# Kernel optimization log

Measured on AMD Instinct MI355X. Metric: run time of the kernel, lower is better.

The kernel has to match this reference:

```python
import jax, jax.numpy as jnp
import numpy as np

B, Q, K, DIM, H = 16, 256, 4096, 1024, 16
HD = DIM // H          # head_dim = 64
SCALE = float(np.sqrt(HD))
MAX_QUERIES = 64       # keep_first=True -> kept Q' = MAX_QUERIES + 1


def setup_inputs() -> dict:
    key = jax.random.key(0)
    ks = jax.random.split(key, 8)
    s = 1.0 / np.sqrt(DIM)
    return {
        "q": jax.random.normal(ks[0], (B, Q, DIM), jnp.float32),
        "k": jax.random.normal(ks[1], (B, K, DIM), jnp.float32),
        "v": jax.random.normal(ks[2], (B, K, DIM), jnp.float32),
        "Wq": jax.random.normal(ks[3], (DIM, DIM), jnp.float32) * s,
        "Wk": jax.random.normal(ks[4], (DIM, DIM), jnp.float32) * s,
        "Wv": jax.random.normal(ks[5], (DIM, DIM), jnp.float32) * s,
        "Wo": jax.random.normal(ks[6], (DIM, DIM), jnp.float32) * s,
        "bo": jnp.zeros((DIM,), jnp.float32),
    }


def _split_heads(x):  # [B, L, DIM] -> [B, L, H, HD]
    return x.reshape(x.shape[0], x.shape[1], H, HD)


def reference(q, k, v, Wq, Wk, Wv, Wo, bo):
    # QKV projections (no bias, matching qkv_bias=False; torch Linear is x @ W.T)
    qh = _split_heads(q @ Wq.T)   # [B,Q,H,HD]
    kh = _split_heads(k @ Wk.T)   # [B,K,H,HD]
    vh = _split_heads(v @ Wv.T)   # [B,K,H,HD]

    dots = jnp.einsum("bqhc,bkhc->bhqk", qh / SCALE, kh)  # [B,H,Q,K]

    # select_queries with keep_first=True: stats on detached dots over queries 1:
    sg = jax.lax.stop_gradient(dots)[:, :, 1:, :]          # [B,H,Q-1,K]
    stats = jax.nn.softmax(sg, axis=-2)                    # softmax over query axis
    score = stats.max(axis=(1, 3))                         # amax over (H, K) -> [B, Q-1]
    _, idx = jax.lax.top_k(score, MAX_QUERIES)             # [B, MAX_QUERIES]
    keep = jnp.concatenate(
        [jnp.zeros((dots.shape[0], 1), idx.dtype), idx + 1], axis=-1
    )                                                      # [B, Q'] with Q' = MAX_QUERIES+1

    dots_sel = jnp.take_along_axis(dots, keep[:, None, :, None], axis=2)  # [B,H,Q',K]

    # Competitive softmax: normalize over the (kept) query axis
    attn = jax.nn.softmax(dots_sel, axis=2)                # [B,H,Q',K]

    out = jnp.einsum("bhqk,bkhc->bqhc", attn, vh)          # [B,Q',H,HD]
    out = out.reshape(out.shape[0], out.shape[1], DIM)     # [B,Q',DIM]
    out = out @ Wo.T + bo
    return out, keep
```

## Files before the change

kernel.cpp:

```cpp
#include <hip/hip_runtime.h>
#include <hip/hip_bf16.h>
#include <math.h>

#define B_ 16
#define Q_ 256
#define K_ 4096
#define DIM_ 1024
#define H_ 16
#define HD_ 64
#define MQ_ 64
#define QP_ 65
#define SCALE_INV 0.125f

typedef unsigned short u16;
typedef __attribute__((ext_vector_type(8))) short bf16x8;
typedef __attribute__((ext_vector_type(8))) _Float16 f16x8;
typedef __attribute__((ext_vector_type(8))) short s16x8;
typedef __attribute__((ext_vector_type(4))) float f32x4;

__device__ __forceinline__ u16 f2bf_rne(float f) {
  unsigned u = __float_as_uint(f);
  u += 0x7fffu + ((u >> 16) & 1u);
  return (u16)(u >> 16);
}
__device__ __forceinline__ float bf2f(u16 h) {
  return __uint_as_float(((unsigned)h) << 16);
}
__device__ __forceinline__ u16 f2h_bits(float f) {
  _Float16 h = (_Float16)f;
  return *(u16*)&h;
}
__device__ __forceinline__ f16x8 as_f16x8(s16x8 v) {
  return __builtin_bit_cast(f16x8, v);
}
__device__ __forceinline__ void gload16(const void* g, void* l) {
  __builtin_amdgcn_global_load_lds(
      (const __attribute__((address_space(1))) unsigned int*)g,
      (__attribute__((address_space(3))) unsigned int*)l, 16, 0, 0);
}

__global__ __launch_bounds__(256) void split_bf16(
    const float* __restrict__ x, u16* __restrict__ hi, u16* __restrict__ lo,
    long n8, int wlo) {
  long i = (long)blockIdx.x * 256 + threadIdx.x;
  const long stride = (long)gridDim.x * 256;
  for (; i < n8; i += stride) {
    const float4 a = ((const float4*)x)[2 * i];
    const float4 b = ((const float4*)x)[2 * i + 1];
    const float xs[8] = {a.x, a.y, a.z, a.w, b.x, b.y, b.z, b.w};
    u16 h[8], l[8];
#pragma unroll
    for (int j = 0; j < 8; ++j) {
      h[j] = f2bf_rne(xs[j]);
      l[j] = f2bf_rne(xs[j] - bf2f(h[j]));
    }
    uint4 hv;
    hv.x = h[0] | ((unsigned)h[1] << 16);
    hv.y = h[2] | ((unsigned)h[3] << 16);
    hv.z = h[4] | ((unsigned)h[5] << 16);
    hv.w = h[6] | ((unsigned)h[7] << 16);
    ((uint4*)hi)[i] = hv;
    if (wlo) {
      uint4 lv;
      lv.x = l[0] | ((unsigned)l[1] << 16);
      lv.y = l[2] | ((unsigned)l[3] << 16);
      lv.z = l[4] | ((unsigned)l[5] << 16);
      lv.w = l[6] | ((unsigned)l[7] << 16);
      ((uint4*)lo)[i] = lv;
    }
  }
}

__global__ __launch_bounds__(256) void split_f16(
    const float* __restrict__ x, u16* __restrict__ hi, u16* __restrict__ lo,
    long n8) {
  long i = (long)blockIdx.x * 256 + threadIdx.x;
  const long stride = (long)gridDim.x * 256;
  for (; i < n8; i += stride) {
    const float4 a = ((const float4*)x)[2 * i];
    const float4 b = ((const float4*)x)[2 * i + 1];
    const float xs[8] = {a.x, a.y, a.z, a.w, b.x, b.y, b.z, b.w};
    u16 h[8], l[8];
#pragma unroll
    for (int j = 0; j < 8; ++j) {
      _Float16 hh = (_Float16)xs[j];
      _Float16 ll = (_Float16)(xs[j] - (float)hh);
      h[j] = *(u16*)&hh;
      l[j] = *(u16*)&ll;
    }
    uint4 hv;
    hv.x = h[0] | ((unsigned)h[1] << 16);
    hv.y = h[2] | ((unsigned)h[3] << 16);
    hv.z = h[4] | ((unsigned)h[5] << 16);
    hv.w = h[6] | ((unsigned)h[7] << 16);
    ((uint4*)hi)[i] = hv;
    uint4 lv;
    lv.x = l[0] | ((unsigned)l[1] << 16);
    lv.y = l[2] | ((unsigned)l[3] << 16);
    lv.z = l[4] | ((unsigned)l[5] << 16);
    lv.w = l[6] | ((unsigned)l[7] << 16);
    ((uint4*)lo)[i] = lv;
  }
}

template <int NPROD, int OUTM>
__global__ __launch_bounds__(256) void mfma_gemm(
    const u16* __restrict__ Ahp, const u16* __restrict__ Alp,
    const u16* __restrict__ Bhp, const u16* __restrict__ Blp,
    float* __restrict__ C, u16* __restrict__ ChH, u16* __restrict__ ChL) {
  __shared__ u16 Ah_s[128 * 32];
  __shared__ u16 Bh_s[128 * 32];
  __shared__ u16 Al_s[NPROD >= 3 ? 128 * 32 : 16];
  __shared__ u16 Bl_s[NPROD >= 3 ? 128 * 32 : 16];
  const int t = threadIdx.x;
  const int wave = t >> 6;
  const int lane = t & 63;
  const int wr = wave >> 1;
  const int wc = wave & 1;

  int bx = blockIdx.x, by = blockIdx.y;
  if (gridDim.x == 8 && (gridDim.y & 7) == 0) {
    const int flat = by * 8 + bx;
    const int c = flat & 7;
    const int j = flat >> 3;
    by = (j >> 3) * 8 + c;
    bx = j & 7;
  }
  const int n0 = bx * 128;
  const int m0 = by * 128;

  const int sr0 = wave * 32 + (lane >> 2);
  const int sr1 = sr0 + 16;
  const int sw0 = ((sr0 ^ (sr0 >> 2)) & 3) ^ (lane & 3);
  const int sw1 = ((sr1 ^ (sr1 >> 2)) & 3) ^ (lane & 3);
  const size_t gA0 = (size_t)(m0 + sr0) * DIM_ + sw0 * 8;
  const size_t gA1 = (size_t)(m0 + sr1) * DIM_ + sw1 * 8;
  const size_t gB0 = (size_t)(n0 + sr0) * DIM_ + sw0 * 8;
  const size_t gB1 = (size_t)(n0 + sr1) * DIM_ + sw1 * 8;
  u16* const lA0 = &Ah_s[(wave * 32) * 32];
  u16* const lA1 = &Ah_s[(wave * 32 + 16) * 32];
  u16* const lB0 = &Bh_s[(wave * 32) * 32];
  u16* const lB1 = &Bh_s[(wave * 32 + 16) * 32];
  u16* const lAl0 = &Al_s[(wave * 32) * 32];
  u16* const lAl1 = &Al_s[(wave * 32 + 16) * 32];
  u16* const lBl0 = &Bl_s[(wave * 32) * 32];
  u16* const lBl1 = &Bl_s[(wave * 32 + 16) * 32];

  int aoff[4], boff[4];
#pragma unroll
  for (int m = 0; m < 4; ++m) {
    const int r = wr * 64 + m * 16 + (lane & 15);
    const int p = ((r ^ (r >> 2)) & 3) ^ (lane >> 4);
    aoff[m] = r * 32 + p * 8;
  }
#pragma unroll
  for (int n = 0; n < 4; ++n) {
    const int r = wc * 64 + n * 16 + (lane & 15);
    const int p = ((r ^ (r >> 2)) & 3) ^ (lane >> 4);
    boff[n] = r * 32 + p * 8;
  }

  f32x4 acc[4][4];
#pragma unroll
  for (int m = 0; m < 4; ++m)
#pragma unroll
    for (int n = 0; n < 4; ++n) acc[m][n] = (f32x4)(0.f);

  for (int k0 = 0; k0 < DIM_; k0 += 32) {
    gload16(Ahp + gA0 + k0, lA0);
    gload16(Ahp + gA1 + k0, lA1);
    gload16(Bhp + gB0 + k0, lB0);
    gload16(Bhp + gB1 + k0, lB1);
    if (NPROD >= 3) {
      gload16(Alp + gA0 + k0, lAl0);
      gload16(Alp + gA1 + k0, lAl1);
      gload16(Blp + gB0 + k0, lBl0);
      gload16(Blp + gB1 + k0, lBl1);
    }
    __syncthreads();
    {
      bf16x8 af[4], bfr[4];
#pragma unroll
      for (int m = 0; m < 4; ++m) af[m] = *(const bf16x8*)&Ah_s[aoff[m]];
#pragma unroll
      for (int n = 0; n < 4; ++n) bfr[n] = *(const bf16x8*)&Bh_s[boff[n]];
#pragma unroll
      for (int m = 0; m < 4; ++m)
#pragma unroll
        for (int n = 0; n < 4; ++n)
          acc[m][n] = __builtin_amdgcn_mfma_f32_16x16x32_bf16(
              af[m], bfr[n], acc[m][n], 0, 0, 0);
      if (NPROD >= 3) {
#pragma unroll
        for (int n = 0; n < 4; ++n) bfr[n] = *(const bf16x8*)&Bl_s[boff[n]];
#pragma unroll
        for (int m = 0; m < 4; ++m)
#pragma unroll
          for (int n = 0; n < 4; ++n)
            acc[m][n] = __builtin_amdgcn_mfma_f32_16x16x32_bf16(
                af[m], bfr[n], acc[m][n], 0, 0, 0);
#pragma unroll
        for (int m = 0; m < 4; ++m) af[m] = *(const bf16x8*)&Al_s[aoff[m]];
#pragma unroll
        for (int n = 0; n < 4; ++n) bfr[n] = *(const bf16x8*)&Bh_s[boff[n]];
#pragma unroll
        for (int m = 0; m < 4; ++m)
#pragma unroll
          for (int n = 0; n < 4; ++n)
            acc[m][n] = __builtin_amdgcn_mfma_f32_16x16x32_bf16(
                af[m], bfr[n], acc[m][n], 0, 0, 0);
      }
    }
    __syncthreads();
  }
#pragma unroll
  for (int m = 0; m < 4; ++m) {
    const int row = m0 + wr * 64 + m * 16 + (lane >> 4) * 4;
#pragma unroll
    for (int n = 0; n < 4; ++n) {
      const int col = n0 + wc * 64 + n * 16 + (lane & 15);
#pragma unroll
      for (int j = 0; j < 4; ++j) {
        const size_t idx = (size_t)(row + j) * DIM_ + col;
        const float a = acc[m][n][j];
        if (OUTM & 1) C[idx] = a;
        if (OUTM & 4) {
          _Float16 hi = (_Float16)a;
          ChH[idx] = *(u16*)&hi;
          if (OUTM & 8) {
            _Float16 lo = (_Float16)(a - (float)hi);
            ChL[idx] = *(u16*)&lo;
          }
        }
      }
    }
  }
}

#define GM 128
#define GN 128
#define GK 16

__global__ __launch_bounds__(256) void gemm_nt(
    const float* __restrict__ A, const float* __restrict__ W,
    float* __restrict__ C, int M, const float* __restrict__ bias) {
  __shared__ float As[GK][GM + 4];
  __shared__ float Ws[GK][GN + 4];
  const int t = threadIdx.x;
  const int m0 = blockIdx.x * GM;
  const int n0 = blockIdx.y * GN;
  const int lrow = t >> 2;
  const int lq = (t & 3) * 4;
  const int tm = (t >> 4) * 8;
  const int tn = (t & 15) * 8;
  float acc[8][8];
#pragma unroll
  for (int i = 0; i < 8; ++i)
#pragma unroll
    for (int j = 0; j < 8; ++j) acc[i][j] = 0.f;

  for (int k0 = 0; k0 < DIM_; k0 += GK) {
#pragma unroll
    for (int half = 0; half < 2; ++half) {
      const int row = lrow + half * 64;
      const int gm = m0 + row;
      float4 av = make_float4(0.f, 0.f, 0.f, 0.f);
      if (gm < M) av = *(const float4*)&A[(size_t)gm * DIM_ + k0 + lq];
      As[lq + 0][row] = av.x; As[lq + 1][row] = av.y;
      As[lq + 2][row] = av.z; As[lq + 3][row] = av.w;
      const int gn = n0 + row;
      const float4 wv = *(const float4*)&W[(size_t)gn * DIM_ + k0 + lq];
      Ws[lq + 0][row] = wv.x; Ws[lq + 1][row] = wv.y;
      Ws[lq + 2][row] = wv.z; Ws[lq + 3][row] = wv.w;
    }
    __syncthreads();
#pragma unroll
    for (int kk = 0; kk < GK; ++kk) {
      float a[8], bb[8];
      *(float4*)&a[0] = *(const float4*)&As[kk][tm];
      *(float4*)&a[4] = *(const float4*)&As[kk][tm + 4];
      *(float4*)&bb[0] = *(const float4*)&Ws[kk][tn];
      *(float4*)&bb[4] = *(const float4*)&Ws[kk][tn + 4];
#pragma unroll
      for (int i = 0; i < 8; ++i)
#pragma unroll
        for (int j = 0; j < 8; ++j)
          acc[i][j] = fmaf(a[i], bb[j], acc[i][j]);
    }
    __syncthreads();
  }
#pragma unroll
  for (int i = 0; i < 8; ++i) {
    const int gm = m0 + tm + i;
    if (gm < M) {
#pragma unroll
      for (int j = 0; j < 8; j += 4) {
        const int gn = n0 + tn + j;
        float4 ov;
        ov.x = acc[i][j + 0]; ov.y = acc[i][j + 1];
        ov.z = acc[i][j + 2]; ov.w = acc[i][j + 3];
        if (bias) {
          ov.x += bias[gn + 0]; ov.y += bias[gn + 1];
          ov.z += bias[gn + 2]; ov.w += bias[gn + 3];
        }
        *(float4*)&C[(size_t)gm * DIM_ + gn] = ov;
      }
    }
  }
}

__device__ __forceinline__ unsigned fflip(float x) {
  const unsigned u = __float_as_uint(x);
  return (u & 0x80000000u) ? ~u : (u | 0x80000000u);
}

#define AKT 64

__global__ __launch_bounds__(256) void pass_a_mfma(
    const u16* __restrict__ qhH, const u16* __restrict__ qhL,
    const u16* __restrict__ khH, const u16* __restrict__ khL,
    unsigned* __restrict__ sbuf) {
  __shared__ u16 KsH[AKT * 72];
  __shared__ u16 KsL[AKT * 72];
  __shared__ float red[4][2 * AKT];
  const int bx = blockIdx.x;
  const int b = bx >> 7;
  const int h = (bx >> 3) & 15;
  const int ks0 = (bx & 7) * (K_ / 8);
  const int t = threadIdx.x;
  const int w = t >> 6;
  const int l = t & 63;
  const int g = l >> 4;
  const int a15 = l & 15;

  f16x8 qA[2][4][2];
#pragma unroll
  for (int mt = 0; mt < 4; ++mt) {
    const int qrow = w * 64 + mt * 16 + a15;
    const size_t base = ((size_t)(b * Q_ + qrow)) * DIM_ + h * HD_;
#pragma unroll
    for (int ks = 0; ks < 2; ++ks) {
      qA[0][mt][ks] = *(const f16x8*)&qhH[base + ks * 32 + g * 8];
      qA[1][mt][ks] = *(const f16x8*)&qhL[base + ks * 32 + g * 8];
    }
  }
  float rmax[4][4];
#pragma unroll
  for (int mt = 0; mt < 4; ++mt)
#pragma unroll
    for (int j = 0; j < 4; ++j) rmax[mt][j] = -3.4e38f;

  for (int k0 = ks0; k0 < ks0 + K_ / 8; k0 += AKT) {
    uint4 sH[2], sL[2];
    int sr[2], sc[2];
#pragma unroll
    for (int s = 0; s < 2; ++s) {
      const int c = t + 256 * s;
      sr[s] = c >> 3;
      sc[s] = c & 7;
      const size_t gidx =
          ((size_t)(b * K_ + k0 + sr[s])) * DIM_ + h * HD_ + sc[s] * 8;
      sH[s] = *(const uint4*)&khH[gidx];
      sL[s] = *(const uint4*)&khL[gidx];
    }
    __syncthreads();
#pragma unroll
    for (int s = 0; s < 2; ++s) {
      *(uint4*)&KsH[sr[s] * 72 + sc[s] * 8] = sH[s];
      *(uint4*)&KsL[sr[s] * 72 + sc[s] * 8] = sL[s];
    }
    __syncthreads();

    f32x4 acc[4][4];
#pragma unroll
    for (int mt = 0; mt < 4; ++mt)
#pragma unroll
      for (int kt = 0; kt < 4; ++kt) acc[mt][kt] = (f32x4)(0.f);
#pragma unroll
    for (int ks = 0; ks < 2; ++ks) {
#pragma unroll
      for (int kt = 0; kt < 4; ++kt) {
        const f16x8 bH =
            *(const f16x8*)&KsH[(kt * 16 + a15) * 72 + ks * 32 + g * 8];
        const f16x8 bL =
            *(const f16x8*)&KsL[(kt * 16 + a15) * 72 + ks * 32 + g * 8];
#pragma unroll
        for (int mt = 0; mt < 4; ++mt) {
          acc[mt][kt] = __builtin_amdgcn_mfma_f32_16x16x32_f16(
              qA[0][mt][ks], bH, acc[mt][kt], 0, 0, 0);
          acc[mt][kt] = __builtin_amdgcn_mfma_f32_16x16x32_f16(
              qA[0][mt][ks], bL, acc[mt][kt], 0, 0, 0);
          acc[mt][kt] = __builtin_amdgcn_mfma_f32_16x16x32_f16(
              qA[1][mt][ks], bH, acc[mt][kt], 0, 0, 0);
        }
      }
    }
#pragma unroll
    for (int mt = 0; mt < 4; ++mt)
#pragma unroll
      for (int kt = 0; kt < 4; ++kt) acc[mt][kt] = acc[mt][kt] * 0.125f;

    float cmax[4];
#pragma unroll
    for (int kt = 0; kt < 4; ++kt) {
      float m = -3.4e38f;
#pragma unroll
      for (int mt = 0; mt < 4; ++mt)
#pragma unroll
        for (int j = 0; j < 4; ++j) {
          const bool ex = (w == 0) & (mt == 0) & (g == 0) & (j == 0);
          if (!ex) m = fmaxf(m, acc[mt][kt][j]);
        }
      m = fmaxf(m, __shfl_xor(m, 16, 64));
      m = fmaxf(m, __shfl_xor(m, 32, 64));
      cmax[kt] = m;
    }
    if (l < 16) {
#pragma unroll
      for (int kt = 0; kt < 4; ++kt) red[w][kt * 16 + l] = cmax[kt];
    }
    __syncthreads();
#pragma unroll
    for (int kt = 0; kt < 4; ++kt)
      cmax[kt] = fmaxf(fmaxf(red[0][kt * 16 + a15], red[1][kt * 16 + a15]),
                       fmaxf(red[2][kt * 16 + a15], red[3][kt * 16 + a15]));
    float csum[4];
#pragma unroll
    for (int kt = 0; kt < 4; ++kt) {
      float s = 0.f;
#pragma unroll
      for (int mt = 0; mt < 4; ++mt)
#pragma unroll
        for (int j = 0; j < 4; ++j) {
          const bool ex = (w == 0) & (mt == 0) & (g == 0) & (j == 0);
          if (!ex) s += __expf(acc[mt][kt][j] - cmax[kt]);
        }
      s += __shfl_xor(s, 16, 64);
      s += __shfl_xor(s, 32, 64);
      csum[kt] = s;
    }
    if (l < 16) {
#pragma unroll
      for (int kt = 0; kt < 4; ++kt) red[w][AKT + kt * 16 + l] = csum[kt];
    }
    __syncthreads();
    float lse[4];
#pragma unroll
    for (int kt = 0; kt < 4; ++kt) {
      const float s = red[0][AKT + kt * 16 + a15] + red[1][AKT + kt * 16 + a15] +
                      red[2][AKT + kt * 16 + a15] + red[3][AKT + kt * 16 + a15];
      lse[kt] = cmax[kt] + logf(s);
    }
#pragma unroll
    for (int mt = 0; mt < 4; ++mt)
#pragma unroll
      for (int j = 0; j < 4; ++j) {
        float v = -3.4e38f;
#pragma unroll
        for (int kt = 0; kt < 4; ++kt)
          v = fmaxf(v, acc[mt][kt][j] - lse[kt]);
        v = fmaxf(v, __shfl_xor(v, 1, 64));
        v = fmaxf(v, __shfl_xor(v, 2, 64));
        v = fmaxf(v, __shfl_xor(v, 4, 64));
        v = fmaxf(v, __shfl_xor(v, 8, 64));
        rmax[mt][j] = fmaxf(rmax[mt][j], v);
      }
  }
  if (a15 == 0) {
#pragma unroll
    for (int mt = 0; mt < 4; ++mt)
#pragma unroll
      for (int j = 0; j < 4; ++j) {
        const int qi = w * 64 + mt * 16 + g * 4 + j;
        if (qi > 0) atomicMax(&sbuf[b * Q_ + qi], fflip(rmax[mt][j]));
      }
  }
}

#define KT 64
#define DC 32
#define KSPLIT 8

__global__ __launch_bounds__(256) void pass_a(
    const float* __restrict__ qh, const float* __restrict__ kh,
    unsigned* __restrict__ sbuf) {
  __shared__ float qs[DC][Q_ + 4];
  __shared__ float ksm[DC][KT + 4];
  __shared__ float red[32][KT + 1];
  __shared__ float cmax[KT];
  __shared__ float clse[KT];
  const int blk = blockIdx.x;
  const int b = blk >> 7;
  const int h = (blk >> 3) & 15;
  const int ks0 = (blk & 7) * (K_ / KSPLIT);
  const int t = threadIdx.x;
  const int tq = t >> 3;
  const int tk = t & 7;
  float rmax[8];
#pragma unroll
  for (int i = 0; i < 8; ++i) rmax[i] = -3.4e38f;

  for (int k0 = ks0; k0 < ks0 + K_ / KSPLIT; k0 += KT) {
    float acc[8][8];
#pragma unroll
    for (int i = 0; i < 8; ++i)
#pragma unroll
      for (int j = 0; j < 8; ++j) acc[i][j] = 0.f;

    for (int dc = 0; dc < HD_; dc += DC) {
      {
        const float* src = &qh[((size_t)(b * Q_ + t)) * DIM_ + h * HD_ + dc];
#pragma unroll
        for (int u = 0; u < DC / 4; ++u) {
          const float4 vv = *(const float4*)&src[u * 4];
          qs[u * 4 + 0][t] = vv.x * SCALE_INV;
          qs[u * 4 + 1][t] = vv.y * SCALE_INV;
          qs[u * 4 + 2][t] = vv.z * SCALE_INV;
          qs[u * 4 + 3][t] = vv.w * SCALE_INV;
        }
      }
      {
        const int r = t >> 2;
        const int qd = (t & 3) * 8;
        const float* src =
            &kh[((size_t)(b * K_ + k0 + r)) * DIM_ + h * HD_ + dc + qd];
#pragma unroll
        for (int u = 0; u < 2; ++u) {
          const float4 vv = *(const float4*)&src[u * 4];
          ksm[qd + u * 4 + 0][r] = vv.x; ksm[qd + u * 4 + 1][r] = vv.y;
          ksm[qd + u * 4 + 2][r] = vv.z; ksm[qd + u * 4 + 3][r] = vv.w;
        }
      }
      __syncthreads();
#pragma unroll
      for (int d = 0; d < DC; ++d) {
        float a[8], bb[8];
        *(float4*)&a[0] = *(const float4*)&qs[d][tq * 8];
        *(float4*)&a[4] = *(const float4*)&qs[d][tq * 8 + 4];
        *(float4*)&bb[0] = *(const float4*)&ksm[d][tk * 8];
        *(float4*)&bb[4] = *(const float4*)&ksm[d][tk * 8 + 4];
#pragma unroll
        for (int i = 0; i < 8; ++i)
#pragma unroll
          for (int j = 0; j < 8; ++j)
            acc[i][j] = fmaf(a[i], bb[j], acc[i][j]);
      }
      __syncthreads();
    }
#pragma unroll
    for (int j = 0; j < 8; ++j) {
      float m = -3.4e38f;
#pragma unroll
      for (int i = 0; i < 8; ++i) {
        if (tq == 0 && i == 0) continue;
        m = fmaxf(m, acc[i][j]);
      }
      red[tq][tk * 8 + j] = m;
    }
    __syncthreads();
    if (t < KT) {
      float m = -3.4e38f;
      for (int g = 0; g < 32; ++g) m = fmaxf(m, red[g][t]);
      cmax[t] = m;
    }
    __syncthreads();
#pragma unroll
    for (int j = 0; j < 8; ++j) {
      const float m = cmax[tk * 8 + j];
      float s = 0.f;
#pragma unroll
      for (int i = 0; i < 8; ++i) {
        if (tq == 0 && i == 0) continue;
        s += __expf(acc[i][j] - m);
      }
      red[tq][tk * 8 + j] = s;
    }
    __syncthreads();
    if (t < KT) {
      float s = 0.f;
      for (int g = 0; g < 32; ++g) s += red[g][t];
      clse[t] = cmax[t] + logf(s);
    }
    __syncthreads();
#pragma unroll
    for (int i = 0; i < 8; ++i) {
      float v = -3.4e38f;
#pragma unroll
      for (int j = 0; j < 8; ++j) v = fmaxf(v, acc[i][j] - clse[tk * 8 + j]);
      v = fmaxf(v, __shfl_xor(v, 1, 64));
      v = fmaxf(v, __shfl_xor(v, 2, 64));
      v = fmaxf(v, __shfl_xor(v, 4, 64));
      rmax[i] = fmaxf(rmax[i], v);
    }
    __syncthreads();
  }
  if (tk == 0) {
#pragma unroll
    for (int i = 0; i < 8; ++i) {
      const int qi = tq * 8 + i;
      if (qi > 0) atomicMax(&sbuf[b * Q_ + qi], fflip(rmax[i]));
    }
  }
}

__global__ void topk_kernel(const unsigned* __restrict__ sbuf,
                            int* __restrict__ keep, float* __restrict__ keepf) {
  const int b = blockIdx.x;
  const int lane = threadIdx.x;
  unsigned long long pk[4];
#pragma unroll
  for (int j = 0; j < 4; ++j) {
    const int q = 1 + lane + 64 * j;
    if (q <= 255) {
      const unsigned s = sbuf[b * Q_ + q];
      pk[j] = (((unsigned long long)s) << 32) | (unsigned)(256 - q);
    } else {
      pk[j] = 0ull;
    }
  }
  if (lane == 0) { keep[b * QP_] = 0; keepf[b * QP_] = 0.f; }
  for (int it = 0; it < MQ_; ++it) {
    unsigned long long best = pk[0];
#pragma unroll
    for (int j = 1; j < 4; ++j) best = (pk[j] > best) ? pk[j] : best;
    for (int m = 1; m < 64; m <<= 1) {
      const unsigned long long o = __shfl_xor(best, m, 64);
      best = (o > best) ? o : best;
    }
    const int q = 256 - (int)(best & 0xffffffffu);
#pragma unroll
    for (int j = 0; j < 4; ++j)
      if (pk[j] == best) pk[j] = 0ull;
    if (lane == 0) {
      keep[b * QP_ + 1 + it] = q;
      keepf[b * QP_ + 1 + it] = (float)q;
    }
  }
}

#define PSPL 4

__global__ __launch_bounds__(256) void pass_b_mfma(
    const float* __restrict__ qh, const u16* __restrict__ khb,
    const u16* __restrict__ vhb, const int* __restrict__ keep,
    float* __restrict__ part) {
  __shared__ __align__(16) char SH[72960];
  u16* const Qs = (u16*)SH;
  u16* const Ks = (u16*)(SH + 11520);
  u16* const Vs = (u16*)(SH + 29952);
  u16* const Ps = (u16*)(SH + 47360);
  float* const osum = (float*)(SH + 11520);

  const int bx = blockIdx.x;
  const int b = bx >> 6;
  const int h = (bx >> 2) & 15;
  const int sp = bx & 3;
  const int t = threadIdx.x;
  const int w = t >> 6;
  const int l = t & 63;
  const int g = l >> 4;
  const int a15 = l & 15;

  for (int idx = t; idx < 80 * 8; idx += 256) {
    const int row = idx >> 3, ch = idx & 7;
    uint4 pk;
    if (row < QP_) {
      const int kq = keep[b * QP_ + row];
      const float* src = &qh[((size_t)(b * Q_ + kq)) * DIM_ + h * HD_ + ch * 8];
      const float4 x0 = *(const float4*)&src[0];
      const float4 x1 = *(const float4*)&src[4];
      pk.x = f2h_bits(x0.x * SCALE_INV) | ((unsigned)f2h_bits(x0.y * SCALE_INV) << 16);
      pk.y = f2h_bits(x0.z * SCALE_INV) | ((unsigned)f2h_bits(x0.w * SCALE_INV) << 16);
      pk.z = f2h_bits(x1.x * SCALE_INV) | ((unsigned)f2h_bits(x1.y * SCALE_INV) << 16);
      pk.w = f2h_bits(x1.z * SCALE_INV) | ((unsigned)f2h_bits(x1.w * SCALE_INV) << 16);
    } else {
      pk = make_uint4(0, 0, 0, 0);
    }
    *(uint4*)&Qs[row * 72 + ch * 8] = pk;
  }
  __syncthreads();

  f32x4 oacc[5][4];
#pragma unroll
  for (int mt = 0; mt < 5; ++mt)
#pragma unroll
    for (int dt = 0; dt < 4; ++dt) oacc[mt][dt] = (f32x4)(0.f);

  const int kt0 = sp * (K_ / PSPL);
  for (int kt = 0; kt < K_ / PSPL; kt += 128) {
    const int k0 = kt0 + kt;
    uint4 kreg[4], vreg[4];
    int srow[4], sch[4];
#pragma unroll
    for (int s = 0; s < 4; ++s) {
      const int c = t + 256 * s;
      srow[s] = c >> 3;
      sch[s] = c & 7;
      const size_t gidx =
          ((size_t)(b * K_ + k0 + srow[s])) * DIM_ + h * HD_ + sch[s] * 8;
      kreg[s] = *(const uint4*)&khb[gidx];
      vreg[s] = *(const uint4*)&vhb[gidx];
    }
    __syncthreads();
#pragma unroll
    for (int s = 0; s < 4; ++s) {
      *(uint4*)&Ks[srow[s] * 72 + sch[s] * 8] = kreg[s];
      uint2 v0; v0.x = vreg[s].x; v0.y = vreg[s].y;
      uint2 v1; v1.x = vreg[s].z; v1.y = vreg[s].w;
      *(uint2*)&Vs[srow[s] * 68 + sch[s] * 8] = v0;
      *(uint2*)&Vs[srow[s] * 68 + sch[s] * 8 + 4] = v1;
    }
    __syncthreads();

    f32x4 S[5][2];
#pragma unroll
    for (int mt = 0; mt < 5; ++mt)
#pragma unroll
      for (int nt = 0; nt < 2; ++nt) S[mt][nt] = (f32x4)(0.f);
#pragma unroll
    for (int kk = 0; kk < 2; ++kk) {
      f16x8 aq[5];
#pragma unroll
      for (int mt = 0; mt < 5; ++mt)
        aq[mt] = *(const f16x8*)&Qs[(mt * 16 + a15) * 72 + kk * 32 + g * 8];
#pragma unroll
      for (int nt = 0; nt < 2; ++nt) {
        const f16x8 bk =
            *(const f16x8*)&Ks[(w * 32 + nt * 16 + a15) * 72 + kk * 32 + g * 8];
#pragma unroll
        for (int mt = 0; mt < 5; ++mt)
          S[mt][nt] = __builtin_amdgcn_mfma_f32_16x16x32_f16(aq[mt], bk,
                                                             S[mt][nt], 0, 0, 0);
      }
    }
#pragma unroll
    for (int nt = 0; nt < 2; ++nt) {
      float m = -3.4e38f;
#pragma unroll
      for (int mt = 0; mt < 5; ++mt)
#pragma unroll
        for (int j = 0; j < 4; ++j) {
          const bool valid = (mt < 4) | ((g == 0) & (j == 0));
          if (valid) m = fmaxf(m, S[mt][nt][j]);
        }
      m = fmaxf(m, __shfl_xor(m, 16, 64));
      m = fmaxf(m, __shfl_xor(m, 32, 64));
      float s = 0.f;
#pragma unroll
      for (int mt = 0; mt < 5; ++mt)
#pragma unroll
        for (int j = 0; j < 4; ++j) {
          const bool valid = (mt < 4) | ((g == 0) & (j == 0));
          const float p = valid ? __expf(S[mt][nt][j] - m) : 0.f;
          S[mt][nt][j] = p;
          s += p;
        }
      s += __shfl_xor(s, 16, 64);
      s += __shfl_xor(s, 32, 64);
      const float r = 1.f / s;
#pragma unroll
      for (int mt = 0; mt < 5; ++mt)
#pragma unroll
        for (int j = 0; j < 4; ++j)
          Ps[w * 3200 + (mt * 16 + g * 4 + j) * 40 + nt * 16 + a15] =
              f2h_bits(S[mt][nt][j] * r);
    }
    f16x8 ap[5];
#pragma unroll
    for (int mt = 0; mt < 5; ++mt)
      ap[mt] = *(const f16x8*)&Ps[w * 3200 + (mt * 16 + a15) * 40 + g * 8];
#pragma unroll
    for (int dt = 0; dt < 4; ++dt) {
      s16x8 bv;
#pragma unroll
      for (int e = 0; e < 8; ++e)
        bv[e] = (short)Vs[(w * 32 + g * 8 + e) * 68 + dt * 16 + a15];
#pragma unroll
      for (int mt = 0; mt < 5; ++mt)
        oacc[mt][dt] = __builtin_amdgcn_mfma_f32_16x16x32_f16(
            ap[mt], as_f16x8(bv), oacc[mt][dt], 0, 0, 0);
    }
  }

#pragma unroll
  for (int dt = 0; dt < 4; ++dt) {
    __syncthreads();
#pragma unroll
    for (int mt = 0; mt < 5; ++mt)
#pragma unroll
      for (int j = 0; j < 4; ++j)
        osum[w * 1360 + (mt * 16 + g * 4 + j) * 17 + a15] = oacc[mt][dt][j];
    __syncthreads();
    for (int idx = t; idx < QP_ * 16; idx += 256) {
      const int q = idx >> 4, c = idx & 15;
      const float sm = osum[q * 17 + c] + osum[1360 + q * 17 + c] +
                       osum[2720 + q * 17 + c] + osum[4080 + q * 17 + c];
      part[(((size_t)sp * B_ + b) * QP_ + q) * DIM_ + h * 64 + dt * 16 + c] = sm;
    }
  }
}

__global__ __launch_bounds__(256) void pass_b(
    const float* __restrict__ qh, const float* __restrict__ kh,
    const float* __restrict__ vh, const int* __restrict__ keep,
    float* __restrict__ part) {
  __shared__ float qs[QP_][HD_ + 4];
  __shared__ float kv[KT][HD_ + 4];
  __shared__ float att[QP_][KT + 4];
  __shared__ float cmax[KT];
  __shared__ float crcp[KT];
  const int bx = blockIdx.x;
  const int b = bx >> 6;
  const int h = (bx >> 2) & 15;
  const int sp = bx & 3;
  const int t = threadIdx.x;

  if (t < QP_) {
    const int kq = keep[b * QP_ + t];
    const float* src = &qh[((size_t)(b * Q_ + kq)) * DIM_ + h * HD_];
#pragma unroll
    for (int u = 0; u < HD_ / 4; ++u) {
      float4 vv = *(const float4*)&src[u * 4];
      vv.x *= SCALE_INV; vv.y *= SCALE_INV;
      vv.z *= SCALE_INV; vv.w *= SCALE_INV;
      *(float4*)&qs[t][u * 4] = vv;
    }
  }
  const int c = t & 63;
  const int jg = t >> 6;
  const int j0 = jg * 17;
  const int j1 = (jg == 3) ? QP_ : (j0 + 17);
  const int j2 = t >> 2;
  const int cg = (t & 3) * 16;
  const int r = t >> 2;
  const int qd = (t & 3) * 16;
  float oacc[16], oacc2[16];
#pragma unroll
  for (int u = 0; u < 16; ++u) { oacc[u] = 0.f; oacc2[u] = 0.f; }

  __syncthreads();

  const int kbeg = sp * (K_ / PSPL);
  const int kend = kbeg + K_ / PSPL;
  for (int k0 = kbeg; k0 < kend; k0 += KT) {
    {
      const float* src = &kh[((size_t)(b * K_ + k0 + r)) * DIM_ + h * HD_ + qd];
#pragma unroll
      for (int u = 0; u < 4; ++u)
        *(float4*)&kv[r][qd + u * 4] = *(const float4*)&src[u * 4];
    }
    __syncthreads();
    {
      float4 kr[16];
#pragma unroll
      for (int u = 0; u < 16; ++u) kr[u] = *(const float4*)&kv[c][u * 4];
      for (int j = j0; j < j1; ++j) {
        float4 s4 = make_float4(0.f, 0.f, 0.f, 0.f);
#pragma unroll
        for (int u = 0; u < 16; ++u) {
          const float4 qv = *(const float4*)&qs[j][u * 4];
          s4.x = fmaf(qv.x, kr[u].x, s4.x);
          s4.y = fmaf(qv.y, kr[u].y, s4.y);
          s4.z = fmaf(qv.z, kr[u].z, s4.z);
          s4.w = fmaf(qv.w, kr[u].w, s4.w);
        }
        att[j][c] = (s4.x + s4.y) + (s4.z + s4.w);
      }
    }
    __syncthreads();
    {
      const float* src = &vh[((size_t)(b * K_ + k0 + r)) * DIM_ + h * HD_ + qd];
#pragma unroll
      for (int u = 0; u < 4; ++u)
        *(float4*)&kv[r][qd + u * 4] = *(const float4*)&src[u * 4];
      if (t < KT) {
        float m = att[0][t];
        for (int j = 1; j < QP_; ++j) m = fmaxf(m, att[j][t]);
        float s = 0.f;
        for (int j = 0; j < QP_; ++j) s += __expf(att[j][t] - m);
        cmax[t] = m;
        crcp[t] = 1.f / s;
      }
    }
    __syncthreads();
    for (int e = t; e < QP_ * KT; e += 256) {
      const int jj = e >> 6;
      const int cc = e & 63;
      att[jj][cc] = __expf(att[jj][cc] - cmax[cc]) * crcp[cc];
    }
    __syncthreads();
    {
      for (int ck = 0; ck < KT; ++ck) {
        const float a = att[j2][ck];
#pragma unroll
        for (int u = 0; u < 4; ++u) {
          const float4 vv = *(const float4*)&kv[ck][cg + u * 4];
          oacc[u * 4 + 0] = fmaf(a, vv.x, oacc[u * 4 + 0]);
          oacc[u * 4 + 1] = fmaf(a, vv.y, oacc[u * 4 + 1]);
          oacc[u * 4 + 2] = fmaf(a, vv.z, oacc[u * 4 + 2]);
          oacc[u * 4 + 3] = fmaf(a, vv.w, oacc[u * 4 + 3]);
        }
      }
      if (t < 4) {
        const int cg2 = t * 16;
        for (int ck = 0; ck < KT; ++ck) {
          const float a = att[64][ck];
#pragma unroll
          for (int u = 0; u < 4; ++u) {
            const float4 vv = *(const float4*)&kv[ck][cg2 + u * 4];
            oacc2[u * 4 + 0] = fmaf(a, vv.x, oacc2[u * 4 + 0]);
            oacc2[u * 4 + 1] = fmaf(a, vv.y, oacc2[u * 4 + 1]);
            oacc2[u * 4 + 2] = fmaf(a, vv.z, oacc2[u * 4 + 2]);
            oacc2[u * 4 + 3] = fmaf(a, vv.w, oacc2[u * 4 + 3]);
          }
        }
      }
    }
    __syncthreads();
  }
  {
    float* dst =
        &part[(((size_t)sp * B_ + b) * QP_ + j2) * DIM_ + h * HD_ + cg];
    *(float4*)&dst[0] = make_float4(oacc[0], oacc[1], oacc[2], oacc[3]);
    *(float4*)&dst[4] = make_float4(oacc[4], oacc[5], oacc[6], oacc[7]);
    *(float4*)&dst[8] = make_float4(oacc[8], oacc[9], oacc[10], oacc[11]);
    *(float4*)&dst[12] = make_float4(oacc[12], oacc[13], oacc[14], oacc[15]);
    if (t < 4) {
      float* dst2 =
          &part[(((size_t)sp * B_ + b) * QP_ + 64) * DIM_ + h * HD_ + t * 16];
      *(float4*)&dst2[0] = make_float4(oacc2[0], oacc2[1], oacc2[2], oacc2[3]);
      *(float4*)&dst2[4] = make_float4(oacc2[4], oacc2[5], oacc2[6], oacc2[7]);
      *(float4*)&dst2[8] = make_float4(oacc2[8], oacc2[9], oacc2[10], oacc2[11]);
      *(float4*)&dst2[12] = make_float4(oacc2[12], oacc2[13], oacc2[14], oacc2[15]);
    }
  }
}

__global__ __launch_bounds__(256) void reduce_part(
    const float* __restrict__ part, float* __restrict__ opre) {
  const long n4 = (long)B_ * QP_ * DIM_ / 4;
  const long i = (long)blockIdx.x * 256 + threadIdx.x;
  if (i >= n4) return;
  float4 s = ((const float4*)part)[i];
#pragma unroll
  for (int sp = 1; sp < PSPL; ++sp) {
    const float4 p = ((const float4*)part)[(long)sp * n4 + i];
    s.x += p.x; s.y += p.y; s.z += p.z; s.w += p.w;
  }
  ((float4*)opre)[i] = s;
}

extern "C" void kernel_launch(void* const* d_in, const int* in_sizes, int n_in,
                              void* d_out, int out_size, void* d_ws, size_t ws_size,
                              hipStream_t stream) {
  const float* q  = (const float*)d_in[0];
  const float* k  = (const float*)d_in[1];
  const float* v  = (const float*)d_in[2];
  const float* Wq = (const float*)d_in[3];
  const float* Wk = (const float*)d_in[4];
  const float* Wv = (const float*)d_in[5];
  const float* Wo = (const float*)d_in[6];
  const float* bo = (const float*)d_in[7];
  float* out = (float*)d_out;

  char* base = (char*)d_ws;
  size_t off = 0;
  auto alloc = [&](size_t bytes) {
    char* p = base + off;
    off = (off + bytes + 255) & ~(size_t)255;
    return (void*)p;
  };
  float* qh   = (float*)alloc((size_t)B_ * Q_ * DIM_ * 4);
  float* opre = (float*)alloc((size_t)B_ * QP_ * DIM_ * 4);
  unsigned* sbuf = (unsigned*)alloc((size_t)B_ * Q_ * 4);
  int* keep   = (int*)alloc((size_t)B_ * QP_ * 4);
  const size_t common_off = off;
  u16* qhH = (u16*)alloc((size_t)B_ * Q_ * DIM_ * 2);
  u16* qhL = (u16*)alloc((size_t)B_ * Q_ * DIM_ * 2);
  u16* khH = (u16*)alloc((size_t)B_ * K_ * DIM_ * 2);
  u16* khL = (u16*)alloc((size_t)B_ * K_ * DIM_ * 2);
  u16* vhH = (u16*)alloc((size_t)B_ * K_ * DIM_ * 2);
  u16* kHi = (u16*)alloc((size_t)B_ * K_ * DIM_ * 2);
  u16* kLo = (u16*)alloc((size_t)B_ * K_ * DIM_ * 2);
  u16* wHi = (u16*)alloc((size_t)DIM_ * DIM_ * 2);
  u16* wLo = (u16*)alloc((size_t)DIM_ * DIM_ * 2);
  const bool big = (off <= ws_size);
  float* keepf = out + (size_t)B_ * QP_ * DIM_;
  const dim3 blk(256);

  hipMemsetAsync(sbuf, 0, B_ * Q_ * sizeof(unsigned), stream);

  if (big) {
    float* part = (float*)kHi;
    const long nKV8 = (long)B_ * K_ * DIM_ / 8;
    const long nW8 = (long)DIM_ * DIM_ / 8;
    const long nQ8 = (long)B_ * Q_ * DIM_ / 8;
    split_bf16<<<2048, blk, 0, stream>>>(k, kHi, kLo, nKV8, 1);
    split_bf16<<<512, blk, 0, stream>>>(Wk, wHi, wLo, nW8, 1);
    mfma_gemm<3, 12><<<dim3(DIM_ / 128, B_ * K_ / 128), blk, 0, stream>>>(
        kHi, kLo, wHi, wLo, nullptr, khH, khL);
    split_bf16<<<2048, blk, 0, stream>>>(v, kHi, nullptr, nKV8, 0);
    split_bf16<<<512, blk, 0, stream>>>(Wv, wHi, nullptr, nW8, 0);
    mfma_gemm<1, 4><<<dim3(DIM_ / 128, B_ * K_ / 128), blk, 0, stream>>>(
        kHi, nullptr, wHi, nullptr, nullptr, vhH, nullptr);
    gemm_nt<<<dim3(B_ * Q_ / GM, DIM_ / GN), blk, 0, stream>>>(
        q, Wq, qh, B_ * Q_, nullptr);
    split_f16<<<512, blk, 0, stream>>>(qh, qhH, qhL, nQ8);
    pass_a_mfma<<<dim3(B_ * H_ * 8), blk, 0, stream>>>(qhH, qhL, khH, khL, sbuf);
    topk_kernel<<<dim3(B_), dim3(64), 0, stream>>>(sbuf, keep, keepf);
    pass_b_mfma<<<dim3(B_ * H_ * PSPL), blk, 0, stream>>>(qh, khH, vhH, keep, part);
    reduce_part<<<dim3((B_ * QP_ * DIM_ / 4 + 255) / 256), blk, 0, stream>>>(part, opre);
    gemm_nt<<<dim3((B_ * QP_ + GM - 1) / GM, DIM_ / GN), blk, 0, stream>>>(
        opre, Wo, out, B_ * QP_, bo);
  } else {
    off = common_off;
    float* kh = (float*)alloc((size_t)B_ * K_ * DIM_ * 4);
    float* vh = (float*)alloc((size_t)B_ * K_ * DIM_ * 4);
    float* part = (float*)alloc((size_t)PSPL * B_ * QP_ * DIM_ * 4);
    gemm_nt<<<dim3(B_ * K_ / GM, DIM_ / GN), blk, 0, stream>>>(k, Wk, kh, B_ * K_, nullptr);
    gemm_nt<<<dim3(B_ * K_ / GM, DIM_ / GN), blk, 0, stream>>>(v, Wv, vh, B_ * K_, nullptr);
    gemm_nt<<<dim3(B_ * Q_ / GM, DIM_ / GN), blk, 0, stream>>>(q, Wq, qh, B_ * Q_, nullptr);
    pass_a<<<dim3(B_ * H_ * KSPLIT), blk, 0, stream>>>(qh, kh, sbuf);
    topk_kernel<<<dim3(B_), dim3(64), 0, stream>>>(sbuf, keep, keepf);
    pass_b<<<dim3(B_ * H_ * PSPL), blk, 0, stream>>>(qh, kh, vh, keep, part);
    reduce_part<<<dim3((B_ * QP_ * DIM_ / 4 + 255) / 256), blk, 0, stream>>>(part, opre);
    gemm_nt<<<dim3((B_ * QP_ + GM - 1) / GM, DIM_ / GN), blk, 0, stream>>>(
        opre, Wo, out, B_ * QP_, bo);
  }
}
```

Measured before the change: 1.501 ms.

## Fuse fp32-to-bf16 split of K/V into projection GEMMs and Q split into epilogue

```diff
diff --git a/kernel.cpp b/kernel.cpp
--- a/kernel.cpp
+++ b/kernel.cpp
@@ -71,41 +71,9 @@
   }
 }
 
-__global__ __launch_bounds__(256) void split_f16(
-    const float* __restrict__ x, u16* __restrict__ hi, u16* __restrict__ lo,
-    long n8) {
-  long i = (long)blockIdx.x * 256 + threadIdx.x;
-  const long stride = (long)gridDim.x * 256;
-  for (; i < n8; i += stride) {
-    const float4 a = ((const float4*)x)[2 * i];
-    const float4 b = ((const float4*)x)[2 * i + 1];
-    const float xs[8] = {a.x, a.y, a.z, a.w, b.x, b.y, b.z, b.w};
-    u16 h[8], l[8];
-#pragma unroll
-    for (int j = 0; j < 8; ++j) {
-      _Float16 hh = (_Float16)xs[j];
-      _Float16 ll = (_Float16)(xs[j] - (float)hh);
-      h[j] = *(u16*)&hh;
-      l[j] = *(u16*)&ll;
-    }
-    uint4 hv;
-    hv.x = h[0] | ((unsigned)h[1] << 16);
-    hv.y = h[2] | ((unsigned)h[3] << 16);
-    hv.z = h[4] | ((unsigned)h[5] << 16);
-    hv.w = h[6] | ((unsigned)h[7] << 16);
-    ((uint4*)hi)[i] = hv;
-    uint4 lv;
-    lv.x = l[0] | ((unsigned)l[1] << 16);
-    lv.y = l[2] | ((unsigned)l[3] << 16);
-    lv.z = l[4] | ((unsigned)l[5] << 16);
-    lv.w = l[6] | ((unsigned)l[7] << 16);
-    ((uint4*)lo)[i] = lv;
-  }
-}
-
 template <int NPROD, int OUTM>
-__global__ __launch_bounds__(256) void mfma_gemm(
-    const u16* __restrict__ Ahp, const u16* __restrict__ Alp,
+__global__ __launch_bounds__(256) void mfma_gemm_f32a(
+    const float* __restrict__ Af,
     const u16* __restrict__ Bhp, const u16* __restrict__ Blp,
     float* __restrict__ C, u16* __restrict__ ChH, u16* __restrict__ ChL) {
   __shared__ u16 Ah_s[128 * 32];
@@ -133,18 +101,19 @@
   const int sr1 = sr0 + 16;
   const int sw0 = ((sr0 ^ (sr0 >> 2)) & 3) ^ (lane & 3);
   const int sw1 = ((sr1 ^ (sr1 >> 2)) & 3) ^ (lane & 3);
-  const size_t gA0 = (size_t)(m0 + sr0) * DIM_ + sw0 * 8;
-  const size_t gA1 = (size_t)(m0 + sr1) * DIM_ + sw1 * 8;
   const size_t gB0 = (size_t)(n0 + sr0) * DIM_ + sw0 * 8;
   const size_t gB1 = (size_t)(n0 + sr1) * DIM_ + sw1 * 8;
-  u16* const lA0 = &Ah_s[(wave * 32) * 32];
-  u16* const lA1 = &Ah_s[(wave * 32 + 16) * 32];
   u16* const lB0 = &Bh_s[(wave * 32) * 32];
   u16* const lB1 = &Bh_s[(wave * 32 + 16) * 32];
-  u16* const lAl0 = &Al_s[(wave * 32) * 32];
-  u16* const lAl1 = &Al_s[(wave * 32 + 16) * 32];
   u16* const lBl0 = &Bl_s[(wave * 32) * 32];
   u16* const lBl1 = &Bl_s[(wave * 32 + 16) * 32];
+
+  const int ar = t >> 1;
+  const int ac0 = (t & 1) * 2;
+  const int swzr = (ar ^ (ar >> 2)) & 3;
+  const int sl0 = (ac0 ^ swzr) * 8;
+  const int sl1 = ((ac0 + 1) ^ swzr) * 8;
+  const size_t gA = (size_t)(m0 + ar) * DIM_ + ac0 * 8;
 
   int aoff[4], boff[4];
 #pragma unroll
@@ -167,15 +136,41 @@
     for (int n = 0; n < 4; ++n) acc[m][n] = (f32x4)(0.f);
 
   for (int k0 = 0; k0 < DIM_; k0 += 32) {
-    gload16(Ahp + gA0 + k0, lA0);
-    gload16(Ahp + gA1 + k0, lA1);
     gload16(Bhp + gB0 + k0, lB0);
     gload16(Bhp + gB1 + k0, lB1);
     if (NPROD >= 3) {
-      gload16(Alp + gA0 + k0, lAl0);
-      gload16(Alp + gA1 + k0, lAl1);
       gload16(Blp + gB0 + k0, lBl0);
       gload16(Blp + gB1 + k0, lBl1);
+    }
+    {
+      const float4 a0 = *(const float4*)&Af[gA + k0];
+      const float4 a1 = *(const float4*)&Af[gA + k0 + 4];
+      const float4 a2 = *(const float4*)&Af[gA + k0 + 8];
+      const float4 a3 = *(const float4*)&Af[gA + k0 + 12];
+      const float xs[16] = {a0.x, a0.y, a0.z, a0.w, a1.x, a1.y, a1.z, a1.w,
+                            a2.x, a2.y, a2.z, a2.w, a3.x, a3.y, a3.z, a3.w};
+      u16 h[16], l[16];
+#pragma unroll
+      for (int j = 0; j < 16; ++j) {
+        h[j] = f2bf_rne(xs[j]);
+        if (NPROD >= 3) l[j] = f2bf_rne(xs[j] - bf2f(h[j]));
+      }
+      uint4 hv0, hv1;
+      hv0.x = h[0] | ((unsigned)h[1] << 16);  hv0.y = h[2] | ((unsigned)h[3] << 16);
+      hv0.z = h[4] | ((unsigned)h[5] << 16);  hv0.w = h[6] | ((unsigned)h[7] << 16);
+      hv1.x = h[8] | ((unsigned)h[9] << 16);  hv1.y = h[10] | ((unsigned)h[11] << 16);
+      hv1.z = h[12] | ((unsigned)h[13] << 16); hv1.w = h[14] | ((unsigned)h[15] << 16);
+      *(uint4*)&Ah_s[ar * 32 + sl0] = hv0;
+      *(uint4*)&Ah_s[ar * 32 + sl1] = hv1;
+      if (NPROD >= 3) {
+        uint4 lv0, lv1;
+        lv0.x = l[0] | ((unsigned)l[1] << 16);  lv0.y = l[2] | ((unsigned)l[3] << 16);
+        lv0.z = l[4] | ((unsigned)l[5] << 16);  lv0.w = l[6] | ((unsigned)l[7] << 16);
+        lv1.x = l[8] | ((unsigned)l[9] << 16);  lv1.y = l[10] | ((unsigned)l[11] << 16);
+        lv1.z = l[12] | ((unsigned)l[13] << 16); lv1.w = l[14] | ((unsigned)l[15] << 16);
+        *(uint4*)&Al_s[ar * 32 + sl0] = lv0;
+        *(uint4*)&Al_s[ar * 32 + sl1] = lv1;
+      }
     }
     __syncthreads();
     {
@@ -243,7 +238,8 @@
 
 __global__ __launch_bounds__(256) void gemm_nt(
     const float* __restrict__ A, const float* __restrict__ W,
-    float* __restrict__ C, int M, const float* __restrict__ bias) {
+    float* __restrict__ C, int M, const float* __restrict__ bias,
+    u16* __restrict__ hiOut, u16* __restrict__ loOut) {
   __shared__ float As[GK][GM + 4];
   __shared__ float Ws[GK][GN + 4];
   const int t = threadIdx.x;
@@ -293,17 +289,35 @@
   for (int i = 0; i < 8; ++i) {
     const int gm = m0 + tm + i;
     if (gm < M) {
+      float vals[8];
+#pragma unroll
+      for (int j = 0; j < 8; ++j) {
+        vals[j] = acc[i][j];
+        if (bias) vals[j] += bias[n0 + tn + j];
+      }
 #pragma unroll
       for (int j = 0; j < 8; j += 4) {
-        const int gn = n0 + tn + j;
         float4 ov;
-        ov.x = acc[i][j + 0]; ov.y = acc[i][j + 1];
-        ov.z = acc[i][j + 2]; ov.w = acc[i][j + 3];
-        if (bias) {
-          ov.x += bias[gn + 0]; ov.y += bias[gn + 1];
-          ov.z += bias[gn + 2]; ov.w += bias[gn + 3];
-        }
-        *(float4*)&C[(size_t)gm * DIM_ + gn] = ov;
+        ov.x = vals[j + 0]; ov.y = vals[j + 1];
+        ov.z = vals[j + 2]; ov.w = vals[j + 3];
+        *(float4*)&C[(size_t)gm * DIM_ + n0 + tn + j] = ov;
+      }
+      if (hiOut) {
+        u16 h[8], l[8];
+#pragma unroll
+        for (int j = 0; j < 8; ++j) {
+          _Float16 hh = (_Float16)vals[j];
+          _Float16 ll = (_Float16)(vals[j] - (float)hh);
+          h[j] = *(u16*)&hh;
+          l[j] = *(u16*)&ll;
+        }
+        uint4 hv, lv;
+        hv.x = h[0] | ((unsigned)h[1] << 16); hv.y = h[2] | ((unsigned)h[3] << 16);
+        hv.z = h[4] | ((unsigned)h[5] << 16); hv.w = h[6] | ((unsigned)h[7] << 16);
+        lv.x = l[0] | ((unsigned)l[1] << 16); lv.y = l[2] | ((unsigned)l[3] << 16);
+        lv.z = l[4] | ((unsigned)l[5] << 16); lv.w = l[6] | ((unsigned)l[7] << 16);
+        *(uint4*)&hiOut[(size_t)gm * DIM_ + n0 + tn] = hv;
+        *(uint4*)&loOut[(size_t)gm * DIM_ + n0 + tn] = lv;
       }
     }
   }
@@ -980,10 +994,9 @@
   u16* khH = (u16*)alloc((size_t)B_ * K_ * DIM_ * 2);
   u16* khL = (u16*)alloc((size_t)B_ * K_ * DIM_ * 2);
   u16* vhH = (u16*)alloc((size_t)B_ * K_ * DIM_ * 2);
-  u16* kHi = (u16*)alloc((size_t)B_ * K_ * DIM_ * 2);
-  u16* kLo = (u16*)alloc((size_t)B_ * K_ * DIM_ * 2);
   u16* wHi = (u16*)alloc((size_t)DIM_ * DIM_ * 2);
   u16* wLo = (u16*)alloc((size_t)DIM_ * DIM_ * 2);
+  float* partBig = (float*)alloc((size_t)PSPL * B_ * QP_ * DIM_ * 4);
   const bool big = (off <= ws_size);
   float* keepf = out + (size_t)B_ * QP_ * DIM_;
   const dim3 blk(256);
@@ -991,40 +1004,37 @@
   hipMemsetAsync(sbuf, 0, B_ * Q_ * sizeof(unsigned), stream);
 
   if (big) {
-    float* part = (float*)kHi;
-    const long nKV8 = (long)B_ * K_ * DIM_ / 8;
     const long nW8 = (long)DIM_ * DIM_ / 8;
-    const long nQ8 = (long)B_ * Q_ * DIM_ / 8;
-    split_bf16<<<2048, blk, 0, stream>>>(k, kHi, kLo, nKV8, 1);
     split_bf16<<<512, blk, 0, stream>>>(Wk, wHi, wLo, nW8, 1);
-    mfma_gemm<3, 12><<<dim3(DIM_ / 128, B_ * K_ / 128), blk, 0, stream>>>(
-        kHi, kLo, wHi, wLo, nullptr, khH, khL);
-    split_bf16<<<2048, blk, 0, stream>>>(v, kHi, nullptr, nKV8, 0);
+    mfma_gemm_f32a<3, 12><<<dim3(DIM_ / 128, B_ * K_ / 128), blk, 0, stream>>>(
+        k, wHi, wLo, nullptr, khH, khL);
     split_bf16<<<512, blk, 0, stream>>>(Wv, wHi, nullptr, nW8, 0);
-    mfma_gemm<1, 4><<<dim3(DIM_ / 128, B_ * K_ / 128), blk, 0, stream>>>(
-        kHi, nullptr, wHi, nullptr, nullptr, vhH, nullptr);
+    mfma_gemm_f32a<1, 4><<<dim3(DIM_ / 128, B_ * K_ / 128), blk, 0, stream>>>(
+        v, wHi, nullptr, nullptr, vhH, nullptr);
     gemm_nt<<<dim3(B_ * Q_ / GM, DIM_ / GN), blk, 0, stream>>>(
-        q, Wq, qh, B_ * Q_, nullptr);
-    split_f16<<<512, blk, 0, stream>>>(qh, qhH, qhL, nQ8);
+        q, Wq, qh, B_ * Q_, nullptr, qhH, qhL);
     pass_a_mfma<<<dim3(B_ * H_ * 8), blk, 0, stream>>>(qhH, qhL, khH, khL, sbuf);
     topk_kernel<<<dim3(B_), dim3(64), 0, stream>>>(sbuf, keep, keepf);
-    pass_b_mfma<<<dim3(B_ * H_ * PSPL), blk, 0, stream>>>(qh, khH, vhH, keep, part);
-    reduce_part<<<dim3((B_ * QP_ * DIM_ / 4 + 255) / 256), blk, 0, stream>>>(part, opre);
+    pass_b_mfma<<<dim3(B_ * H_ * PSPL), blk, 0, stream>>>(qh, khH, vhH, keep, partBig);
+    reduce_part<<<dim3((B_ * QP_ * DIM_ / 4 + 255) / 256), blk, 0, stream>>>(partBig, opre);
     gemm_nt<<<dim3((B_ * QP_ + GM - 1) / GM, DIM_ / GN), blk, 0, stream>>>(
-        opre, Wo, out, B_ * QP_, bo);
+        opre, Wo, out, B_ * QP_, bo, nullptr, nullptr);
   } else {
     off = common_off;
     float* kh = (float*)alloc((size_t)B_ * K_ * DIM_ * 4);
     float* vh = (float*)alloc((size_t)B_ * K_ * DIM_ * 4);
     float* part = (float*)alloc((size_t)PSPL * B_ * QP_ * DIM_ * 4);
-    gemm_nt<<<dim3(B_ * K_ / GM, DIM_ / GN), blk, 0, stream>>>(k, Wk, kh, B_ * K_, nullptr);
-    gemm_nt<<<dim3(B_ * K_ / GM, DIM_ / GN), blk, 0, stream>>>(v, Wv, vh, B_ * K_, nullptr);
-    gemm_nt<<<dim3(B_ * Q_ / GM, DIM_ / GN), blk, 0, stream>>>(q, Wq, qh, B_ * Q_, nullptr);
+    gemm_nt<<<dim3(B_ * K_ / GM, DIM_ / GN), blk, 0, stream>>>(
+        k, Wk, kh, B_ * K_, nullptr, nullptr, nullptr);
+    gemm_nt<<<dim3(B_ * K_ / GM, DIM_ / GN), blk, 0, stream>>>(
+        v, Wv, vh, B_ * K_, nullptr, nullptr, nullptr);
+    gemm_nt<<<dim3(B_ * Q_ / GM, DIM_ / GN), blk, 0, stream>>>(
+        q, Wq, qh, B_ * Q_, nullptr, nullptr, nullptr);
     pass_a<<<dim3(B_ * H_ * KSPLIT), blk, 0, stream>>>(qh, kh, sbuf);
     topk_kernel<<<dim3(B_), dim3(64), 0, stream>>>(sbuf, keep, keepf);
     pass_b<<<dim3(B_ * H_ * PSPL), blk, 0, stream>>>(qh, kh, vh, keep, part);
     reduce_part<<<dim3((B_ * QP_ * DIM_ / 4 + 255) / 256), blk, 0, stream>>>(part, opre);
     gemm_nt<<<dim3((B_ * QP_ + GM - 1) / GM, DIM_ / GN), blk, 0, stream>>>(
-        opre, Wo, out, B_ * QP_, bo);
-  }
-}
+        opre, Wo, out, B_ * QP_, bo, nullptr, nullptr);
+  }
+}
```

New measurement: 1.510 ms. About the same (+0.6%).
